# Optimization experiments

Measured on AMD Instinct MI355X. Metric: run time of the kernel, lower is better.

## Reference

```python
import jax, jax.numpy as jnp
import numpy as np

N_HEADS = 16
HEAD_DIM = 64
ROPE_BASE = 10000.0


def _apply_rope(x, offset):
    # x: (B, T, H, hd); rotates consecutive pairs (x[2i], x[2i+1]) as complex numbers,
    # matching torch.view_as_complex on reshape(..., -1, 2).
    B, T, H, hd = x.shape
    inv_freq = 1.0 / (ROPE_BASE ** (jnp.arange(0, hd, 2, dtype=jnp.float32) / hd))  # (hd/2,)
    t = jnp.arange(T, dtype=jnp.float32) + offset
    ang = t[:, None] * inv_freq[None, :]                      # (T, hd/2)
    cos = jnp.cos(ang)[None, :, None, :]                      # (1, T, 1, hd/2)
    sin = jnp.sin(ang)[None, :, None, :]
    x1 = x[..., 0::2]
    x2 = x[..., 1::2]
    out = jnp.stack([x1 * cos - x2 * sin, x1 * sin + x2 * cos], axis=-1)
    return out.reshape(B, T, H, hd).astype(x.dtype)


def setup_inputs() -> dict:
    key = jax.random.key(0)
    ks = jax.random.split(key, 5)
    D = N_HEADS * HEAD_DIM  # 1024
    s = 1.0 / np.sqrt(D)
    x = jax.random.normal(ks[0], (2, 2048, D), jnp.float32)
    Wqkv = jax.random.normal(ks[1], (D, 3 * D), jnp.float32) * s
    bqkv = jax.random.normal(ks[2], (3 * D,), jnp.float32) * 0.01
    Wout = jax.random.normal(ks[3], (D, D), jnp.float32) * s
    bout = jax.random.normal(ks[4], (D,), jnp.float32) * 0.01
    return {"x": x, "Wqkv": Wqkv, "bqkv": bqkv, "Wout": Wout, "bout": bout, "offset": 0}


def reference(x, Wqkv, bqkv, Wout, bout, offset):
    B, T, D = x.shape
    qkv = (x @ Wqkv + bqkv).reshape(B, T, 3, N_HEADS, HEAD_DIM)
    q, k, v = qkv[:, :, 0], qkv[:, :, 1], qkv[:, :, 2]       # (B, T, H, hd)
    q = _apply_rope(q, offset)
    k = _apply_rope(k, offset)
    # kv_cache is None and T == window_size, so no crop occurs.
    new_cache = jnp.stack([k, v], axis=1)                     # (B, 2, T, H, hd)
    scale = 1.0 / np.sqrt(HEAD_DIM)
    scores = jnp.einsum("bqhd,bkhd->bhqk", q, k) * scale      # (B, H, T, T)
    mask = jnp.tril(jnp.ones((T, T), dtype=bool))
    scores = jnp.where(mask[None, None], scores, jnp.finfo(scores.dtype).min)
    attn = jax.nn.softmax(scores, axis=-1)
    ctx = jnp.einsum("bhqk,bkhd->bqhd", attn, v).reshape(B, T, D)
    out = ctx @ Wout + bout
    return (out, new_cache)
```

## Files before the change

### kernel.cpp

```cpp
#include <hip/hip_runtime.h>
#include <stdint.h>
#include <math.h>


typedef __bf16 bf16_t;
typedef bf16_t bf16x8 __attribute__((ext_vector_type(8)));
typedef float f32x4 __attribute__((ext_vector_type(4)));
typedef unsigned short ushort8_t __attribute__((ext_vector_type(8)));

__device__ __forceinline__ unsigned short f2bf(float f) {
    union { float f; unsigned int i; } v; v.f = f;
    unsigned int r = v.i + 0x7fffu + ((v.i >> 16) & 1u);
    return (unsigned short)(r >> 16);
}
__device__ __forceinline__ bf16x8 ld8(const unsigned short* p) {
    return *(const bf16x8*)p;
}
__device__ __forceinline__ void gload_lds16(const unsigned short* g, unsigned short* l) {
    __builtin_amdgcn_global_load_lds(
        (__attribute__((address_space(1))) void*)(g),
        (__attribute__((address_space(3))) void*)(l),
        16, 0, 0);
}

__global__ void k_cvt(const float* __restrict__ in, unsigned short* __restrict__ out) {
    const int i = (blockIdx.x * 256 + threadIdx.x) * 8;
    float4 a = *(const float4*)&in[i];
    float4 b = *(const float4*)&in[i + 4];
    ushort8_t v;
    v[0] = f2bf(a.x); v[1] = f2bf(a.y); v[2] = f2bf(a.z); v[3] = f2bf(a.w);
    v[4] = f2bf(b.x); v[5] = f2bf(b.y); v[6] = f2bf(b.z); v[7] = f2bf(b.w);
    *(ushort8_t*)&out[i] = v;
}

__global__ void k_ropetab(float* __restrict__ tab, const int* __restrict__ offp) {
    int idx = blockIdx.x * blockDim.x + threadIdx.x;
    int t = idx >> 5, i = idx & 31;
    float off = (float)(*offp);
    float inv = powf(10000.0f, -(float)(2 * i) / 64.0f);
    float ang = ((float)t + off) * inv;
    float s, c;
    sincosf(ang, &s, &c);
    tab[idx * 2]     = c;
    tab[idx * 2 + 1] = s;
}

__global__ void k_transposeF2B(const float* __restrict__ in,
                               unsigned short* __restrict__ out, int R, int C) {
    __shared__ __align__(16) float tile[64 * 68];
    const int bz = blockIdx.z;
    const size_t base = (size_t)bz * R * C;
    const int tR = blockIdx.y * 64, tC = blockIdx.x * 64;
    const int tid = threadIdx.x;
#pragma unroll
    for (int it = 0; it < 4; ++it) {
        int flat = (it * 256 + tid) * 4;
        int r = flat >> 6, c = flat & 63;
        *(float4*)&tile[r * 68 + c] =
            *(const float4*)&in[base + (size_t)(tR + r) * C + tC + c];
    }
    __syncthreads();
#pragma unroll
    for (int it = 0; it < 2; ++it) {
        int flat = (it * 256 + tid) * 8;
        int rr = flat >> 6, cc = flat & 63;
        ushort8_t v;
#pragma unroll
        for (int j = 0; j < 8; ++j) v[j] = f2bf(tile[(cc + j) * 68 + rr]);
        *(ushort8_t*)&out[base + (size_t)(tC + rr) * R + tR + cc] = v;
    }
}

__global__ void k_transpose64(const unsigned short* __restrict__ in,
                              unsigned short* __restrict__ out, int R, int C) {
    __shared__ __align__(16) unsigned short tile[64 * 72];
    const int bz = blockIdx.z;
    const size_t base = (size_t)bz * R * C;
    const int tR = blockIdx.y * 64, tC = blockIdx.x * 64;
    const int tid = threadIdx.x;
#pragma unroll
    for (int it = 0; it < 2; ++it) {
        int flat = (it * 256 + tid) * 8;
        int r = flat >> 6, c = flat & 63;
        *(ushort8_t*)&tile[r * 72 + c] =
            *(const ushort8_t*)&in[base + (size_t)(tR + r) * C + tC + c];
    }
    __syncthreads();
#pragma unroll
    for (int it = 0; it < 2; ++it) {
        int flat = (it * 256 + tid) * 8;
        int rr = flat >> 6, cc = flat & 63;
        ushort8_t v;
#pragma unroll
        for (int j = 0; j < 8; ++j) v[j] = tile[(cc + j) * 72 + rr];
        *(ushort8_t*)&out[base + (size_t)(tC + rr) * R + tR + cc] = v;
    }
}

template <int EPI>
__global__ __launch_bounds__(256) void k_gemm(
    const unsigned short* __restrict__ A,
    const unsigned short* __restrict__ Bt,
    const float* __restrict__ bias,
    const float* __restrict__ tab,
    unsigned short* __restrict__ oq,
    unsigned short* __restrict__ ok,
    unsigned short* __restrict__ ov,
    float* __restrict__ cache,
    float* __restrict__ outp)
{
    constexpr int K = 1024;
    __shared__ __align__(16) unsigned short lA[2][128 * 32];
    __shared__ __align__(16) unsigned short lB[2][128 * 32];
    const int tid = threadIdx.x;
    const int wave = tid >> 6, lane = tid & 63;
    const int lrow = lane & 15, quad = lane >> 4;
    const int waveM = wave >> 1, waveN = wave & 1;
    const int blockM = blockIdx.y * 128, blockN = blockIdx.x * 128;

    f32x4 acc[4][4];
#pragma unroll
    for (int i = 0; i < 4; ++i)
#pragma unroll
        for (int j = 0; j < 4; ++j) acc[i][j] = (f32x4){0.f, 0.f, 0.f, 0.f};

    auto stage = [&](int k0, int bsel) {
#pragma unroll
        for (int it = 0; it < 2; ++it) {
            int flat = (it * 256 + tid) * 8;
            gload_lds16(&A[(size_t)(blockM + (flat >> 5)) * K + k0 + (flat & 31)],
                        &lA[bsel][it * 2048 + wave * 512]);
            gload_lds16(&Bt[(size_t)(blockN + (flat >> 5)) * K + k0 + (flat & 31)],
                        &lB[bsel][it * 2048 + wave * 512]);
        }
    };

    stage(0, 0);
    int buf = 0;
    for (int k0 = 0; k0 < K; k0 += 32) {
        __syncthreads();
        if (k0 + 32 < K) stage(k0 + 32, buf ^ 1);
        bf16x8 af[4], bfr[4];
#pragma unroll
        for (int mt = 0; mt < 4; ++mt)
            af[mt] = ld8(&lA[buf][(waveM * 64 + mt * 16 + lrow) * 32 + quad * 8]);
#pragma unroll
        for (int nt = 0; nt < 4; ++nt)
            bfr[nt] = ld8(&lB[buf][(waveN * 64 + nt * 16 + lrow) * 32 + quad * 8]);
#pragma unroll
        for (int mt = 0; mt < 4; ++mt)
#pragma unroll
            for (int nt = 0; nt < 4; ++nt)
                acc[mt][nt] = __builtin_amdgcn_mfma_f32_16x16x32_bf16(
                    af[mt], bfr[nt], acc[mt][nt], 0, 0, 0);
        buf ^= 1;
    }

#pragma unroll
    for (int mt = 0; mt < 4; ++mt) {
        const int rbase = blockM + waveM * 64 + mt * 16 + quad * 4;
#pragma unroll
        for (int nt = 0; nt < 4; ++nt) {
            const int gcol = blockN + waveN * 64 + nt * 16 + lrow;
            const float bv = bias[gcol];
#pragma unroll
            for (int r = 0; r < 4; ++r) {
                const int row = rbase + r;
                float val = acc[mt][nt][r] + bv;
                if (EPI == 0) {
                    outp[(size_t)row * 1024 + gcol] = val;
                } else {
                    const int s = gcol >> 10;
                    const int cn = gcol & 1023;
                    const int h = cn >> 6, d = cn & 63;
                    const int b = row >> 11, t = row & 2047;
                    if (s < 2) {
                        const int i = d >> 1;
                        const float cz = tab[t * 64 + 2 * i];
                        const float sz = tab[t * 64 + 2 * i + 1];
                        const float pv = __shfl_xor(val, 1);
                        val = (d & 1) ? (pv * sz + val * cz) : (val * cz - pv * sz);
                    }
                    const unsigned short r16 = f2bf(val);
                    const size_t bhtd = (((size_t)(b * 16 + h)) * 2048 + t) * 64 + d;
                    if (s == 0) {
                        oq[bhtd] = r16;
                    } else if (s == 1) {
                        ok[bhtd] = r16;
                        cache[(((size_t)(b * 2 + 0)) * 2048 + t) * 1024 + h * 64 + d] = val;
                    } else {
                        ov[bhtd] = r16;
                        cache[(((size_t)(b * 2 + 1)) * 2048 + t) * 1024 + h * 64 + d] = val;
                    }
                }
            }
        }
    }
}

__global__ __launch_bounds__(256, 3) void k_attn(
    const unsigned short* __restrict__ qh,
    const unsigned short* __restrict__ kh,
    const unsigned short* __restrict__ vt,
    unsigned short* __restrict__ ctx)
{
    __shared__ __align__(16) unsigned short lK[2][64 * 64];
    __shared__ __align__(16) unsigned short lV[2][64 * 64];
    __shared__ __align__(16) unsigned short lP[4][32 * 68];
    const int tid = threadIdx.x;
    const int wave = tid >> 6, lane = tid & 63;
    const int lrow = lane & 15, quad = lane >> 4;
    const int sub = lane >> 3, g8 = lane & 7;
    const int grp = g8 ^ (sub & 7);
    const int pj = blockIdx.x;
    const int h = blockIdx.y, b = blockIdx.z;
    const unsigned short* Q  = qh + (size_t)(b * 16 + h) * 2048 * 64;
    const unsigned short* Kp = kh + (size_t)(b * 16 + h) * 2048 * 64;
    const unsigned short* Vt = vt + (size_t)(b * 16 + h) * 64 * 2048;

    bf16x8 bOnes;
#pragma unroll
    for (int j = 0; j < 8; ++j) bOnes[j] = (bf16_t)1.0f;

    for (int phase = 0; phase < 2; ++phase) {
        const int qb = phase ? pj : (15 - pj);
        const int qw = qb * 128 + wave * 32;

        bf16x8 aQ[2][2];
#pragma unroll
        for (int mf = 0; mf < 2; ++mf)
#pragma unroll
            for (int ks = 0; ks < 2; ++ks) {
                bf16x8 t = ld8(&Q[(size_t)(qw + mf * 16 + lrow) * 64 + ks * 32 + quad * 8]);
#pragma unroll
                for (int j = 0; j < 8; ++j) t[j] = (bf16_t)((float)t[j] * 0.125f);
                aQ[mf][ks] = t;
            }

        f32x4 o[2][4];
#pragma unroll
        for (int mf = 0; mf < 2; ++mf)
#pragma unroll
            for (int i = 0; i < 4; ++i) o[mf][i] = (f32x4){0.f, 0.f, 0.f, 0.f};
        f32x4 lacc[2];
        lacc[0] = (f32x4){0.f, 0.f, 0.f, 0.f};
        lacc[1] = (f32x4){0.f, 0.f, 0.f, 0.f};

        const int nT = 2 * (qb + 1);

        __syncthreads();
#pragma unroll
        for (int i = 0; i < 2; ++i) {
            const int c = wave * 2 + i;
            gload_lds16(&Kp[(size_t)(c * 8 + sub) * 64 + grp * 8], &lK[0][c * 512]);
            gload_lds16(&Vt[(size_t)(c * 8 + sub) * 2048 + grp * 8], &lV[0][c * 512]);
        }

        int buf = 0;
        for (int it = 0; it < nT; ++it) {
            const int kt0 = it * 64;
            __syncthreads();
            if (it + 1 < nT) {
                const int kn = kt0 + 64;
#pragma unroll
                for (int i = 0; i < 2; ++i) {
                    const int c = wave * 2 + i;
                    gload_lds16(&Kp[(size_t)(kn + c * 8 + sub) * 64 + grp * 8], &lK[buf ^ 1][c * 512]);
                    gload_lds16(&Vt[(size_t)(c * 8 + sub) * 2048 + kn + grp * 8], &lV[buf ^ 1][c * 512]);
                }
            }
            if (kt0 < qw + 32) {
                const unsigned short* lKb = lK[buf];
                const unsigned short* lVb = lV[buf];
                f32x4 s[2][4];
#pragma unroll
                for (int mf = 0; mf < 2; ++mf)
#pragma unroll
                    for (int i = 0; i < 4; ++i) s[mf][i] = (f32x4){0.f, 0.f, 0.f, 0.f};
#pragma unroll
                for (int nt = 0; nt < 4; ++nt) {
                    const int row = nt * 16 + lrow;
#pragma unroll
                    for (int ks = 0; ks < 2; ++ks) {
                        bf16x8 bK = ld8(&lKb[row * 64 + (((ks * 4 + quad) ^ (row & 7)) * 8)]);
#pragma unroll
                        for (int mf = 0; mf < 2; ++mf)
                            s[mf][nt] = __builtin_amdgcn_mfma_f32_16x16x32_bf16(
                                aQ[mf][ks], bK, s[mf][nt], 0, 0, 0);
                    }
                }
                if (kt0 + 63 > qw) {
#pragma unroll
                    for (int mf = 0; mf < 2; ++mf)
#pragma unroll
                        for (int nt = 0; nt < 4; ++nt) {
                            const int colg = kt0 + nt * 16 + lrow;
#pragma unroll
                            for (int r = 0; r < 4; ++r) {
                                const int rowg = qw + mf * 16 + quad * 4 + r;
                                const float pv = (colg <= rowg) ? __expf(s[mf][nt][r]) : 0.f;
                                lP[wave][(mf * 16 + quad * 4 + r) * 68 + nt * 16 + lrow] = f2bf(pv);
                            }
                        }
                } else {
#pragma unroll
                    for (int mf = 0; mf < 2; ++mf)
#pragma unroll
                        for (int nt = 0; nt < 4; ++nt)
#pragma unroll
                            for (int r = 0; r < 4; ++r)
                                lP[wave][(mf * 16 + quad * 4 + r) * 68 + nt * 16 + lrow] =
                                    f2bf(__expf(s[mf][nt][r]));
                }
                bf16x8 aP[2][2];
#pragma unroll
                for (int mf = 0; mf < 2; ++mf)
#pragma unroll
                    for (int ks = 0; ks < 2; ++ks)
                        aP[mf][ks] = ld8(&lP[wave][(mf * 16 + lrow) * 68 + ks * 32 + quad * 8]);
#pragma unroll
                for (int mf = 0; mf < 2; ++mf)
#pragma unroll
                    for (int ks = 0; ks < 2; ++ks)
                        lacc[mf] = __builtin_amdgcn_mfma_f32_16x16x32_bf16(
                            aP[mf][ks], bOnes, lacc[mf], 0, 0, 0);
#pragma unroll
                for (int dt = 0; dt < 4; ++dt) {
                    const int row = dt * 16 + lrow;
#pragma unroll
                    for (int ks = 0; ks < 2; ++ks) {
                        bf16x8 bV = ld8(&lVb[row * 64 + (((ks * 4 + quad) ^ (row & 7)) * 8)]);
#pragma unroll
                        for (int mf = 0; mf < 2; ++mf)
                            o[mf][dt] = __builtin_amdgcn_mfma_f32_16x16x32_bf16(
                                aP[mf][ks], bV, o[mf][dt], 0, 0, 0);
                    }
                }
            }
            buf ^= 1;
        }

        float inv[2][4];
#pragma unroll
        for (int mf = 0; mf < 2; ++mf)
#pragma unroll
            for (int r = 0; r < 4; ++r) inv[mf][r] = 1.0f / lacc[mf][r];
#pragma unroll
        for (int mf = 0; mf < 2; ++mf)
#pragma unroll
            for (int dt = 0; dt < 4; ++dt) {
                const int col = h * 64 + dt * 16 + lrow;
#pragma unroll
                for (int r = 0; r < 4; ++r) {
                    const int trow = qw + mf * 16 + quad * 4 + r;
                    ctx[((size_t)(b * 2048 + trow)) * 1024 + col] = f2bf(o[mf][dt][r] * inv[mf][r]);
                }
            }
    }
}

extern "C" void kernel_launch(void* const* d_in, const int* in_sizes, int n_in,
                              void* d_out, int out_size, void* d_ws, size_t ws_size,
                              hipStream_t stream) {
    (void)in_sizes; (void)n_in; (void)out_size; (void)ws_size;
    const float* x    = (const float*)d_in[0];
    const float* wqkv = (const float*)d_in[1];
    const float* bqkv = (const float*)d_in[2];
    const float* wout = (const float*)d_in[3];
    const float* bout = (const float*)d_in[4];
    const int*   offp = (const int*)d_in[5];

    float* out   = (float*)d_out;
    float* cache = out + (size_t)2 * 2048 * 1024;

    char* w = (char*)d_ws;
    float* tab            = (float*)w;          w += (size_t)2048 * 64 * sizeof(float);
    unsigned short* xb    = (unsigned short*)w; w += (size_t)4194304 * 2;
    unsigned short* wqkvT = (unsigned short*)w; w += (size_t)3072 * 1024 * 2;
    unsigned short* woutT = (unsigned short*)w; w += (size_t)1024 * 1024 * 2;
    unsigned short* qh    = (unsigned short*)w; w += (size_t)4194304 * 2;
    unsigned short* kh    = (unsigned short*)w; w += (size_t)4194304 * 2;
    unsigned short* vh    = (unsigned short*)w; w += (size_t)4194304 * 2;
    unsigned short* vt    = (unsigned short*)w; w += (size_t)4194304 * 2;
    unsigned short* ctx   = (unsigned short*)w; w += (size_t)4194304 * 2;

    k_ropetab<<<dim3(256), dim3(256), 0, stream>>>(tab, offp);
    k_cvt<<<dim3(2048), dim3(256), 0, stream>>>(x, xb);
    k_transposeF2B<<<dim3(48, 16, 1), dim3(256), 0, stream>>>(wqkv, wqkvT, 1024, 3072);
    k_transposeF2B<<<dim3(16, 16, 1), dim3(256), 0, stream>>>(wout, woutT, 1024, 1024);
    k_gemm<1><<<dim3(24, 32), dim3(256), 0, stream>>>(xb, wqkvT, bqkv, tab, qh, kh, vh, cache, nullptr);
    k_transpose64<<<dim3(1, 32, 32), dim3(256), 0, stream>>>(vh, vt, 2048, 64);
    k_attn<<<dim3(8, 16, 2), dim3(256), 0, stream>>>(qh, kh, vt, ctx);
    k_gemm<0><<<dim3(8, 32), dim3(256), 0, stream>>>(ctx, woutT, bout, tab, nullptr, nullptr, nullptr, nullptr, out);
}
```

Measured before the change: 242.9 us.

## Rewrite GEMM as 256x256 tile, 8-wave, 4-slot pipelined kernel with swizzled LDS

Replaces the 128x128 double-buffered GEMM with a 256x256 tile kernel using 512 threads, a 4-slot LDS ring of 64-wide K chunks, XOR-swizzled LDS layout, and fine-grained interleaving of global-to-LDS loads with MFMA phases guarded by vmcnt waits and barriers. It also adds a block-index swizzle for L2 locality and raises MFMA priority with setprio. The aim is more data reuse per tile and better overlap of memory with compute. In exchange the grids become small (192 and 64 blocks) on a 256-CU device, which can leave CUs idle, and the register pressure is higher.

```diff
diff --git a/kernel.cpp b/kernel.cpp
--- a/kernel.cpp
+++ b/kernel.cpp
@@ -98,7 +98,7 @@
 }
 
 template <int EPI>
-__global__ __launch_bounds__(256) void k_gemm(
+__global__ __launch_bounds__(512, 2) void k_gemm(
     const unsigned short* __restrict__ A,
     const unsigned short* __restrict__ Bt,
     const float* __restrict__ bias,
@@ -110,63 +110,111 @@
     float* __restrict__ outp)
 {
     constexpr int K = 1024;
-    __shared__ __align__(16) unsigned short lA[2][128 * 32];
-    __shared__ __align__(16) unsigned short lB[2][128 * 32];
-    const int tid = threadIdx.x;
-    const int wave = tid >> 6, lane = tid & 63;
+    constexpr int NT = 16;
+    __shared__ __align__(16) unsigned short lds[65536];
+    unsigned short* lA = lds;
+    unsigned short* lB = lds + 32768;
+
+    const int tid  = threadIdx.x;
+    const int lane = tid & 63, w = tid >> 6;
+    const int wr = w >> 2, wc = w & 3;
     const int lrow = lane & 15, quad = lane >> 4;
-    const int waveM = wave >> 1, waveN = wave & 1;
-    const int blockM = blockIdx.y * 128, blockN = blockIdx.x * 128;
-
-    f32x4 acc[4][4];
-#pragma unroll
-    for (int i = 0; i < 4; ++i)
-#pragma unroll
-        for (int j = 0; j < 4; ++j) acc[i][j] = (f32x4){0.f, 0.f, 0.f, 0.f};
-
-    auto stage = [&](int k0, int bsel) {
-#pragma unroll
-        for (int it = 0; it < 2; ++it) {
-            int flat = (it * 256 + tid) * 8;
-            gload_lds16(&A[(size_t)(blockM + (flat >> 5)) * K + k0 + (flat & 31)],
-                        &lA[bsel][it * 2048 + wave * 512]);
-            gload_lds16(&Bt[(size_t)(blockN + (flat >> 5)) * K + k0 + (flat & 31)],
-                        &lB[bsel][it * 2048 + wave * 512]);
+
+    const int gx  = gridDim.x;
+    const int nwg = gx * gridDim.y;
+    const int bid = blockIdx.y * gx + blockIdx.x;
+    const int sw  = (bid & 7) * (nwg >> 3) + (bid >> 3);
+    const int blockM = (sw / gx) * 256;
+    const int blockN = (sw % gx) * 256;
+
+    const int q8    = (lane & 7) ^ (lane >> 3);
+    const int srow0 = ((w * 16 + (lane >> 3)) << 1) + ((q8 >> 2) & 1);
+    const int scol  = (q8 & 3) * 8;
+    const unsigned short* srcA = A  + (size_t)(blockM + srow0) * K + scol;
+    const unsigned short* srcB = Bt + (size_t)(blockN + srow0) * K + scol;
+    unsigned short* dA = lA + w * 1024;
+    unsigned short* dB = lB + w * 1024;
+
+    const int rp   = lrow >> 1;
+    const int swzu = ((((lane & 1) << 6) | (quad << 4)) ^ (rp << 4)) >> 1;
+
+    f32x4 acc[8][4];
+#pragma unroll
+    for (int m = 0; m < 8; ++m)
+#pragma unroll
+        for (int n = 0; n < 4; ++n) acc[m][n] = (f32x4){0.f, 0.f, 0.f, 0.f};
+
+#define STAGE_A(T, KH) do { \
+        const unsigned short* s_ = srcA + (T) * 64 + (KH) * 32; \
+        unsigned short* d_ = dA + (((2*(T)+(KH)) & 3) << 13); \
+        gload_lds16(s_, d_); \
+        gload_lds16(s_ + 16 * K, d_ + 512); } while (0)
+#define STAGE_B(T, KH) do { \
+        const unsigned short* s_ = srcB + (T) * 64 + (KH) * 32; \
+        unsigned short* d_ = dB + (((2*(T)+(KH)) & 3) << 13); \
+        gload_lds16(s_, d_); \
+        gload_lds16(s_ + 16 * K, d_ + 512); } while (0)
+
+    STAGE_A(0, 0); STAGE_B(0, 0);
+    STAGE_A(0, 1); STAGE_B(0, 1);
+    STAGE_A(1, 0); STAGE_B(1, 0);
+    asm volatile("s_waitcnt vmcnt(8)" ::: "memory");
+    __builtin_amdgcn_s_barrier();
+
+    bf16x8 aA[8], bB[2];
+    for (int i = 0; i < NT / 2; ++i) {
+        const int E = 2 * i, O = 2 * i + 1;
+#pragma unroll
+        for (int p = 0; p < 8; ++p) {
+            const int T    = (p < 4) ? E : O;
+            const int ks   = (p >> 1) & 1;
+            const int nh   = p & 1;
+            const int slot = (2 * T + ks) & 3;
+            asm volatile("s_waitcnt vmcnt(6)" ::: "memory");
+            if (nh == 0) {
+#pragma unroll
+                for (int m = 0; m < 8; ++m)
+                    aA[m] = ld8(&lA[(slot << 13) + (wr * 64 + m * 8 + rp) * 64 + swzu]);
+            }
+#pragma unroll
+            for (int nl = 0; nl < 2; ++nl)
+                bB[nl] = ld8(&lB[(slot << 13) + (wc * 32 + nh * 16 + nl * 8 + rp) * 64 + swzu]);
+            if      (p == 0) { STAGE_A(O, 1); }
+            else if (p == 1) { STAGE_B(O, 1); }
+            else if (p == 2) { if (E + 2 < NT) STAGE_A(E + 2, 0); }
+            else if (p == 3) { if (E + 2 < NT) STAGE_B(E + 2, 0); }
+            else if (p == 4) { if (E + 2 < NT) STAGE_A(E + 2, 1); }
+            else if (p == 5) { if (E + 2 < NT) STAGE_B(E + 2, 1); }
+            else if (p == 6) { if (O + 2 < NT) STAGE_A(O + 2, 0); }
+            else             { if (O + 2 < NT) STAGE_B(O + 2, 0); }
+            __builtin_amdgcn_s_barrier();
+            asm volatile("s_waitcnt lgkmcnt(0)" ::: "memory");
+            __builtin_amdgcn_sched_barrier(0);
+            __builtin_amdgcn_s_setprio(1);
+#pragma unroll
+            for (int m = 0; m < 8; ++m)
+#pragma unroll
+                for (int nl = 0; nl < 2; ++nl)
+                    acc[m][nh * 2 + nl] = __builtin_amdgcn_mfma_f32_16x16x32_bf16(
+                        aA[m], bB[nl], acc[m][nh * 2 + nl], 0, 0, 0);
+            __builtin_amdgcn_s_setprio(0);
+            __builtin_amdgcn_s_barrier();
         }
-    };
-
-    stage(0, 0);
-    int buf = 0;
-    for (int k0 = 0; k0 < K; k0 += 32) {
-        __syncthreads();
-        if (k0 + 32 < K) stage(k0 + 32, buf ^ 1);
-        bf16x8 af[4], bfr[4];
-#pragma unroll
-        for (int mt = 0; mt < 4; ++mt)
-            af[mt] = ld8(&lA[buf][(waveM * 64 + mt * 16 + lrow) * 32 + quad * 8]);
-#pragma unroll
-        for (int nt = 0; nt < 4; ++nt)
-            bfr[nt] = ld8(&lB[buf][(waveN * 64 + nt * 16 + lrow) * 32 + quad * 8]);
-#pragma unroll
-        for (int mt = 0; mt < 4; ++mt)
-#pragma unroll
-            for (int nt = 0; nt < 4; ++nt)
-                acc[mt][nt] = __builtin_amdgcn_mfma_f32_16x16x32_bf16(
-                    af[mt], bfr[nt], acc[mt][nt], 0, 0, 0);
-        buf ^= 1;
-    }
-
-#pragma unroll
-    for (int mt = 0; mt < 4; ++mt) {
-        const int rbase = blockM + waveM * 64 + mt * 16 + quad * 4;
-#pragma unroll
-        for (int nt = 0; nt < 4; ++nt) {
-            const int gcol = blockN + waveN * 64 + nt * 16 + lrow;
+    }
+#undef STAGE_A
+#undef STAGE_B
+
+#pragma unroll
+    for (int m = 0; m < 8; ++m) {
+        const int rbase = blockM + wr * 128 + m * 16 + quad * 4;
+#pragma unroll
+        for (int n = 0; n < 4; ++n) {
+            const int gcol = blockN + wc * 64 + n * 16 + lrow;
             const float bv = bias[gcol];
 #pragma unroll
             for (int r = 0; r < 4; ++r) {
                 const int row = rbase + r;
-                float val = acc[mt][nt][r] + bv;
+                float val = acc[m][n][r] + bv;
                 if (EPI == 0) {
                     outp[(size_t)row * 1024 + gcol] = val;
                 } else {
@@ -175,9 +223,9 @@
                     const int h = cn >> 6, d = cn & 63;
                     const int b = row >> 11, t = row & 2047;
                     if (s < 2) {
-                        const int i = d >> 1;
-                        const float cz = tab[t * 64 + 2 * i];
-                        const float sz = tab[t * 64 + 2 * i + 1];
+                        const int ii = d >> 1;
+                        const float cz = tab[t * 64 + 2 * ii];
+                        const float sz = tab[t * 64 + 2 * ii + 1];
                         const float pv = __shfl_xor(val, 1);
                         val = (d & 1) ? (pv * sz + val * cz) : (val * cz - pv * sz);
                     }
@@ -388,8 +436,8 @@
     k_cvt<<<dim3(2048), dim3(256), 0, stream>>>(x, xb);
     k_transposeF2B<<<dim3(48, 16, 1), dim3(256), 0, stream>>>(wqkv, wqkvT, 1024, 3072);
     k_transposeF2B<<<dim3(16, 16, 1), dim3(256), 0, stream>>>(wout, woutT, 1024, 1024);
-    k_gemm<1><<<dim3(24, 32), dim3(256), 0, stream>>>(xb, wqkvT, bqkv, tab, qh, kh, vh, cache, nullptr);
+    k_gemm<1><<<dim3(12, 16), dim3(512), 0, stream>>>(xb, wqkvT, bqkv, tab, qh, kh, vh, cache, nullptr);
     k_transpose64<<<dim3(1, 32, 32), dim3(256), 0, stream>>>(vh, vt, 2048, 64);
     k_attn<<<dim3(8, 16, 2), dim3(256), 0, stream>>>(qh, kh, vt, ctx);
-    k_gemm<0><<<dim3(8, 32), dim3(256), 0, stream>>>(ctx, woutT, bout, tab, nullptr, nullptr, nullptr, nullptr, out);
-}
+    k_gemm<0><<<dim3(4, 16), dim3(512), 0, stream>>>(ctx, woutT, bout, tab, nullptr, nullptr, nullptr, nullptr, out);
+}
```

Result: slower. 258.1 us (+6.3%).
